# Performance work log

Hardware: AMD Instinct MI355X
Metric: run time of the kernel (lower is better)

The kernel has to match this reference:

```python
import jax, jax.numpy as jnp
import numpy as np

KS = (7, 7)
ST = (3, 3)
PD = (3, 3)
DIM = 512
HID = 1960  # 40 * 49, divisible by kernel_shape


def _patch_flat_idx(out_h, out_w):
    kh, kw = KS; sh, sw = ST; ph, pw = PD
    oh = (out_h + 2 * ph - kh) // sh + 1
    ow = (out_w + 2 * pw - kw) // sw + 1
    Wp = out_w + 2 * pw
    iy = jnp.arange(kh)[:, None, None, None] + (jnp.arange(oh) * sh)[None, None, :, None]
    ix = jnp.arange(kw)[None, :, None, None] + (jnp.arange(ow) * sw)[None, None, None, :]
    # (kh, kw, oh, ow) flat index into padded image
    return (iy * Wp + ix), oh, ow


def fold(patches, out_h, out_w):
    # patches: (B, C*kh*kw, L) -> (B, C, out_h, out_w), overlap-add like F.fold
    kh, kw = KS; ph, pw = PD
    idx, oh, ow = _patch_flat_idx(out_h, out_w)
    B, CK, L = patches.shape
    C = CK // (kh * kw)
    Hp, Wp = out_h + 2 * ph, out_w + 2 * pw
    p = patches.reshape(B, C, kh, kw, oh, ow)
    out = jnp.zeros((B, C, Hp * Wp), patches.dtype)
    out = out.at[:, :, idx.reshape(-1)].add(p.reshape(B, C, -1))
    return out.reshape(B, C, Hp, Wp)[:, :, ph:ph + out_h, pw:pw + out_w]


def unfold(img, out_h, out_w):
    # img: (B, C, H, W) -> (B, C*kh*kw, L), like F.unfold
    kh, kw = KS; ph, pw = PD
    idx, oh, ow = _patch_flat_idx(out_h, out_w)
    B, C = img.shape[:2]
    imgp = jnp.pad(img, ((0, 0), (0, 0), (ph, ph), (pw, pw)))
    flat = imgp.reshape(B, C, -1)
    g = flat[:, :, idx.reshape(-1)].reshape(B, C, kh, kw, oh, ow)
    return g.reshape(B, C * kh * kw, oh * ow)


def setup_inputs() -> dict:
    key = jax.random.key(0)
    k1, k2, k3, k4, k5 = jax.random.split(key, 5)
    x = jax.random.normal(k1, (2, 5760, DIM), dtype=jnp.float32)
    W1 = jax.random.normal(k2, (HID, DIM), dtype=jnp.float32) * 0.02
    b1 = jax.random.normal(k3, (HID,), dtype=jnp.float32) * 0.02
    W2 = jax.random.normal(k4, (DIM, HID), dtype=jnp.float32) * 0.02
    b2 = jax.random.normal(k5, (DIM,), dtype=jnp.float32) * 0.02
    return {"x": x, "W1": W1, "b1": b1, "W2": W2, "b2": b2, "out_h": 60, "out_w": 108}


def reference(x, W1, b1, W2, b2, out_h, out_w):
    kh, kw = KS; sh, sw = ST; ph, pw = PD
    oh = (out_h + 2 * ph - kh) // sh + 1
    ow = (out_w + 2 * pw - kw) // sw + 1
    n_vecs = oh * ow
    h = jnp.einsum('bnd,hd->bnh', x, W1) + b1          # (b, n, HID)
    b_, n, c = h.shape
    p = h.reshape(-1, n_vecs, c).transpose(0, 2, 1)     # (B', c, L)
    folded = fold(p, out_h, out_w)                      # (B', c//49, H, W)
    ones = jnp.ones((p.shape[0], kh * kw, n_vecs), h.dtype)
    norm = fold(ones, out_h, out_w)                     # (B', 1, H, W)
    y = unfold(folded / norm, out_h, out_w)             # (B', c, L)
    y = y.transpose(0, 2, 1).reshape(b_, n, c)
    out = jnp.einsum('bnh,dh->bnd', jax.nn.gelu(y, approximate=False), W2) + b2
    return out
```

## Files before the change

### kernel.cpp

```cpp
#include <hip/hip_runtime.h>
#include <cmath>

#define M_ROWS   11520
#define DIM      512
#define HID      1960
#define HIDP     2048
#define KP2      1984
#define OH       20
#define OW       36
#define LVEC     720
#define NCH      40
#define BPRIME   16
#define HP       66
#define WP       114

typedef unsigned short u16;
typedef __bf16 bf16x8 __attribute__((ext_vector_type(8)));
typedef float  f32x4  __attribute__((ext_vector_type(4)));

__device__ __forceinline__ u16 f2bf(float f) {
    unsigned u = __float_as_uint(f);
    u += 0x7fffu + ((u >> 16) & 1u);
    return (u16)(u >> 16);
}
__device__ __forceinline__ float bf2f(u16 h) {
    return __uint_as_float(((unsigned)h) << 16);
}

__device__ __forceinline__ void gload_lds16(const void* g, void* l) {
    __builtin_amdgcn_global_load_lds(
        (const __attribute__((address_space(1))) void*)g,
        (__attribute__((address_space(3))) void*)l, 16, 0, 0);
}

#define CVT_XB   5760
#define CVT_W1B  1024
#define CVT_W2B  1024
#define CVT_Z    270
__global__ __launch_bounds__(256) void cvt_all(const float* __restrict__ x,
                                               const float* __restrict__ W1,
                                               const float* __restrict__ W2,
                                               u16* __restrict__ xb,
                                               u16* __restrict__ W1b,
                                               u16* __restrict__ W2b,
                                               u16* __restrict__ g2) {
    const int b = blockIdx.x;
    const int tid = threadIdx.x;
    ushort4 o;
    if (b < CVT_XB) {
        int i = (b * 256 + tid) * 4;
        float4 v = *(const float4*)(x + i);
        o.x = f2bf(v.x); o.y = f2bf(v.y); o.z = f2bf(v.z); o.w = f2bf(v.w);
        *(ushort4*)(xb + i) = o;
    } else if (b < CVT_XB + CVT_W1B) {
        int i = ((b - CVT_XB) * 256 + tid) * 4;
        if (i < HID * DIM) {
            float4 v = *(const float4*)(W1 + i);
            o.x = f2bf(v.x); o.y = f2bf(v.y); o.z = f2bf(v.z); o.w = f2bf(v.w);
        } else {
            o.x = o.y = o.z = o.w = 0;
        }
        *(ushort4*)(W1b + i) = o;
    } else if (b < CVT_XB + CVT_W1B + CVT_W2B) {
        int i = ((b - CVT_XB - CVT_W1B) * 256 + tid) * 4;
        int d = i / HIDP, c = i - d * HIDP;
        if (c < HID) {
            float4 v = *(const float4*)(W2 + (size_t)d * HID + c);
            o.x = f2bf(v.x); o.y = f2bf(v.y); o.z = f2bf(v.z); o.w = f2bf(v.w);
        } else {
            o.x = o.y = o.z = o.w = 0;
        }
        *(ushort4*)(W2b + i) = o;
    } else {
        int i = ((b - CVT_XB - CVT_W1B - CVT_W2B) * 256 + tid) * 4;
        int row = i / 24, c = i - row * 24;
        o.x = o.y = o.z = o.w = 0;
        *(ushort4*)(g2 + (size_t)row * HIDP + HID + c) = o;
    }
}

template <int OUT_BF16, int BM, int BN>
__global__ __launch_bounds__(512) void gemm_bt(const u16* __restrict__ A,
                                               const u16* __restrict__ B,
                                               const float* __restrict__ bias,
                                               int biasN, void* __restrict__ Cout,
                                               int N, int K, int ldk) {
    constexpr int WM = BM / 4;
    constexpr int WN = BN / 2;
    constexpr int MU = WM / 16;
    constexpr int NU = WN / 16;
    constexpr int ACH = BM * 8;
    constexpr int BCH = BN * 8;

    __shared__ u16 sA[BM * 64];
    __shared__ u16 sB[BN * 64];

    const int tid  = threadIdx.x;
    const int ntn  = N / BN;
    const int NB   = gridDim.x;
    const int v    = (blockIdx.x & 7) * (NB >> 3) + (blockIdx.x >> 3);
    const int bm   = v / ntn;
    const int bn   = v - bm * ntn;
    const int lane = tid & 63;
    const int wv   = tid >> 6;
    const int wm   = (wv >> 1) * WM;
    const int wn   = (wv & 1) * WN;
    const int r    = lane & 15;
    const int quad = lane >> 4;

    const size_t Arow0 = (size_t)bm * BM * ldk;
    const size_t Brow0 = (size_t)bn * BN * ldk;

    f32x4 acc[MU][NU] = {};

    for (int kt = 0; kt < K; kt += 64) {
        __syncthreads();
#pragma unroll
        for (int i = 0; i < ACH / 512; i++) {
            int e   = i * 512 + tid;
            int row = e >> 3;
            int cp  = e & 7;
            int cg  = cp ^ (row & 7);
            gload_lds16(A + Arow0 + (size_t)row * ldk + kt + cg * 8, (char*)sA + e * 16);
        }
#pragma unroll
        for (int i = 0; i < BCH / 512; i++) {
            int e   = i * 512 + tid;
            int row = e >> 3;
            int cp  = e & 7;
            int cg  = cp ^ (row & 7);
            gload_lds16(B + Brow0 + (size_t)row * ldk + kt + cg * 8, (char*)sB + e * 16);
        }
        __syncthreads();
#pragma unroll
        for (int kk = 0; kk < 2; kk++) {
            bf16x8 af[MU], bg[NU];
#pragma unroll
            for (int t = 0; t < MU; t++) {
                int row = wm + t * 16 + r;
                int c   = (kk * 4 + quad) ^ (row & 7);
                af[t] = *(const bf16x8*)(sA + row * 64 + c * 8);
            }
#pragma unroll
            for (int u = 0; u < NU; u++) {
                int row = wn + u * 16 + r;
                int c   = (kk * 4 + quad) ^ (row & 7);
                bg[u] = *(const bf16x8*)(sB + row * 64 + c * 8);
            }
#pragma unroll
            for (int t = 0; t < MU; t++)
#pragma unroll
                for (int u = 0; u < NU; u++)
                    acc[t][u] = __builtin_amdgcn_mfma_f32_16x16x32_bf16(
                        af[t], bg[u], acc[t][u], 0, 0, 0);
        }
    }

    const int gm0 = bm * BM + wm;
    const int gn0 = bn * BN + wn;
#pragma unroll
    for (int u = 0; u < NU; u++) {
        int gn = gn0 + u * 16 + r;
        float bv = (gn < biasN) ? bias[gn] : 0.0f;
#pragma unroll
        for (int t = 0; t < MU; t++) {
            int gm = gm0 + t * 16 + quad * 4;
#pragma unroll
            for (int q = 0; q < 4; q++) {
                float v2 = acc[t][u][q] + bv;
                if (OUT_BF16)
                    ((u16*)Cout)[(size_t)(gm + q) * N + gn] = f2bf(v2);
                else
                    ((float*)Cout)[(size_t)(gm + q) * N + gn] = v2;
            }
        }
    }
}

__global__ __launch_bounds__(512) void mid_fused(const u16* __restrict__ hg,
                                                 u16* __restrict__ g2) {
    __shared__ u16 sh[12 * 20 * 56];
    __shared__ u16 sG[34 * 58];

    const int b   = blockIdx.x;
    const int bp  = b / (NCH * 4);
    const int rr  = b - bp * (NCH * 4);
    const int ch  = rr >> 2;
    const int s   = (rr >> 1) & 1;
    const int xh  = rr & 1;
    const int o0  = s * 10;
    const int lo  = s * 8;
    const int ox0 = xh * 16;
    const int n0  = bp * LVEC;
    const int c0  = ch * 49;
    const int c0f = c0 & ~7;
    const int koff = c0 & 7;
    const int tid = threadIdx.x;

    {
        const char* hb = (const char*)(hg + (size_t)(n0 + lo * 36 + ox0) * HIDP + c0f);
        for (int t = tid; t < 12 * 20 * 7; t += 512) {
            int r   = (int)(((unsigned)t * 74899u) >> 19);
            int c   = t - r * 7;
            int loy = (int)(((unsigned)r * 3277u) >> 16);
            int oxl = r - 20 * loy;
            gload_lds16(hb + (size_t)(loy * 36 + oxl) * (HIDP * 2) + c * 16,
                        (char*)sh + t * 16);
        }
    }
    __syncthreads();

    const int pxl = tid & 63;
    const int rg  = tid >> 6;
    if (pxl < 58) {
        const int  pxg  = pxl + 54 * xh;
        const bool pxin = (pxg >= 3) && (pxg <= 110);
        const int  kx0  = pxg % 3;
        int  ct[3];
        bool vx[3];
        int  cx = 0;
#pragma unroll
        for (int dx = 0; dx < 3; dx++) {
            int kx = kx0 + 3 * dx, rx = pxg - kx;
            bool ok = pxin && (kx <= 6) && (rx >= 0) && (rx <= 105);
            vx[dx] = ok;
            ct[dx] = ok ? ((rx / 3) - ox0) * 56 + kx : 0;
            cx += ok ? 1 : 0;
        }
        const float fcx = (cx == 3) ? (1.0f / 3.0f) : ((cx == 2) ? 0.5f : 1.0f);

        for (int pr = rg; pr < 34; pr += 8) {
            int py = 3 * o0 + pr;
            float val = 0.0f;
            if (pxin && py >= 3 && py <= 62) {
                int ky0 = py % 3;
                float sum = 0.0f;
                int cy = 0;
#pragma unroll
                for (int dy = 0; dy < 3; dy++) {
                    int ky = ky0 + 3 * dy, ry = py - ky;
                    if (ky <= 6 && ry >= 0 && ry <= 57) {
                        int rt = (ry / 3 - lo) * (20 * 56) + ky * 7 + koff;
                        cy++;
                        float v0 = bf2f(sh[rt + ct[0]]);
                        float v1 = bf2f(sh[rt + ct[1]]);
                        float v2 = bf2f(sh[rt + ct[2]]);
                        sum += vx[0] ? v0 : 0.0f;
                        sum += vx[1] ? v1 : 0.0f;
                        sum += vx[2] ? v2 : 0.0f;
                    }
                }
                float fcy = (cy == 3) ? (1.0f / 3.0f) : ((cy == 2) ? 0.5f : 1.0f);
                float m = sum * fcx * fcy;
                val = 0.5f * m * (1.0f + erff(m * 0.70710678118654752f));
            }
            sG[pr * 58 + pxl] = f2bf(val);
        }
    }
    __syncthreads();

    {
        u16* g2row = g2 + (size_t)(n0 + o0 * 36 + 18 * xh) * HIDP + c0;
        for (int j = tid; j < 10 * 18 * 49; j += 512) {
            int l2 = (int)(((unsigned)j * 42800u) >> 21);
            int k  = j - l2 * 49;
            int oy = (int)(((unsigned)l2 * 57u) >> 10);
            int ox = l2 - 18 * oy;
            int ky = (int)(((unsigned)k * 37u) >> 8);
            int kx = k - 7 * ky;
            g2row[(size_t)(oy * 36 + ox) * HIDP + k] =
                sG[(3 * oy + ky) * 58 + 3 * ox + kx];
        }
    }
}

extern "C" void kernel_launch(void* const* d_in, const int* in_sizes, int n_in,
                              void* d_out, int out_size, void* d_ws, size_t ws_size,
                              hipStream_t stream) {
    (void)in_sizes; (void)n_in; (void)out_size; (void)ws_size;
    const float* x  = (const float*)d_in[0];
    const float* W1 = (const float*)d_in[1];
    const float* b1 = (const float*)d_in[2];
    const float* W2 = (const float*)d_in[3];
    const float* b2 = (const float*)d_in[4];
    float* out = (float*)d_out;

    char* ws = (char*)d_ws;
    u16* xb  = (u16*)(ws);
    u16* W1b = (u16*)(ws + 11796480);
    u16* W2b = (u16*)(ws + 13893632);
    u16* hg  = (u16*)(ws + 15990784);
    u16* g2  = (u16*)(ws + 63176704);

    cvt_all<<<CVT_XB + CVT_W1B + CVT_W2B + CVT_Z, 256, 0, stream>>>(
        x, W1, W2, xb, W1b, W2b, g2);

    gemm_bt<1, 256, 128><<<(M_ROWS / 256) * (HIDP / 128), 512, 0, stream>>>(
        xb, W1b, b1, HID, (void*)hg, HIDP, DIM, DIM);

    mid_fused<<<BPRIME * NCH * 4, 512, 0, stream>>>(hg, g2);

    gemm_bt<0, 128, 64><<<(M_ROWS / 128) * (DIM / 64), 512, 0, stream>>>(
        g2, W2b, b2, DIM, (void*)out, DIM, KP2, HIDP);
}
```

Before: 191.7 us.

## Pipeline GEMM tile loads with a triple-buffered LDS ring and staged bf16 stores

Replaces the single-buffered GEMM with a three-slot LDS ring that issues global-to-LDS loads two tiles ahead and uses explicit vmcnt waits, so loads overlap MFMA work. The first GEMM switches to a BK=32 tile with a different XOR swizzle, and the second keeps BK=64. The bf16 output path now goes through an LDS bounce buffer so each thread writes 16-byte vector stores instead of scattered 2-byte ones. The costs are more LDS per block, hand-counted vmcnt values that assume exactly three loads per thread, and an added occupancy hint in the launch bounds.

```diff
diff --git a/kernel.cpp b/kernel.cpp
--- a/kernel.cpp
+++ b/kernel.cpp
@@ -17,6 +17,7 @@
 typedef unsigned short u16;
 typedef __bf16 bf16x8 __attribute__((ext_vector_type(8)));
 typedef float  f32x4  __attribute__((ext_vector_type(4)));
+typedef unsigned short u16x8 __attribute__((ext_vector_type(8)));
 
 __device__ __forceinline__ u16 f2bf(float f) {
     unsigned u = __float_as_uint(f);
@@ -31,6 +32,12 @@
     __builtin_amdgcn_global_load_lds(
         (const __attribute__((address_space(1))) void*)g,
         (__attribute__((address_space(3))) void*)l, 16, 0, 0);
+}
+
+__device__ __forceinline__ void wg_barrier() {
+    asm volatile("" ::: "memory");
+    __builtin_amdgcn_s_barrier();
+    asm volatile("" ::: "memory");
 }
 
 #define CVT_XB   5760
@@ -79,21 +86,25 @@
     }
 }
 
-template <int OUT_BF16, int BM, int BN>
-__global__ __launch_bounds__(512) void gemm_bt(const u16* __restrict__ A,
-                                               const u16* __restrict__ B,
-                                               const float* __restrict__ bias,
-                                               int biasN, void* __restrict__ Cout,
-                                               int N, int K, int ldk) {
-    constexpr int WM = BM / 4;
-    constexpr int WN = BN / 2;
-    constexpr int MU = WM / 16;
-    constexpr int NU = WN / 16;
-    constexpr int ACH = BM * 8;
-    constexpr int BCH = BN * 8;
-
-    __shared__ u16 sA[BM * 64];
-    __shared__ u16 sB[BN * 64];
+template <int OUT_BF16, int BM, int BN, int BK>
+__global__ __launch_bounds__(512, 4) void gemm_ring(const u16* __restrict__ A,
+                                                    const u16* __restrict__ B,
+                                                    const float* __restrict__ bias,
+                                                    int biasN, void* __restrict__ Cout,
+                                                    int N, int K, int ldk) {
+    constexpr int WM  = BM / 4;
+    constexpr int WN  = BN / 2;
+    constexpr int MU  = WM / 16;
+    constexpr int NU  = WN / 16;
+    constexpr int KB  = BK / 32;
+    constexpr int CPR = BK / 8;
+    constexpr int CA  = BM * CPR;
+    constexpr int CB  = BN * CPR;
+    constexpr int TILEU = (BM + BN) * BK;
+    static_assert(CA % 512 == 0 && CB % 512 == 0, "chunk split");
+    static_assert(CA / 512 + CB / 512 == 3, "need 3 loads/thread for vmcnt(6/3/0)");
+
+    __shared__ u16 smem[3 * TILEU];
 
     const int tid  = threadIdx.x;
     const int ntn  = N / BN;
@@ -110,68 +121,114 @@
 
     const size_t Arow0 = (size_t)bm * BM * ldk;
     const size_t Brow0 = (size_t)bn * BN * ldk;
+    const int NT = K / BK;
+
+    auto issue = [&](int t) {
+        const size_t kt = (size_t)t * BK;
+        u16* sa = smem + (t % 3) * TILEU;
+        u16* sb = sa + BM * BK;
+#pragma unroll
+        for (int i = 0; i < CA / 512; i++) {
+            int e   = i * 512 + tid;
+            int row = e / CPR;
+            int cp  = e % CPR;
+            int key = (BK == 64) ? (row & 7) : ((row >> 1) & 3);
+            gload_lds16(A + Arow0 + (size_t)row * ldk + kt + (size_t)((cp ^ key) * 8),
+                        (char*)sa + e * 16);
+        }
+#pragma unroll
+        for (int i = 0; i < CB / 512; i++) {
+            int e   = i * 512 + tid;
+            int row = e / CPR;
+            int cp  = e % CPR;
+            int key = (BK == 64) ? (row & 7) : ((row >> 1) & 3);
+            gload_lds16(B + Brow0 + (size_t)row * ldk + kt + (size_t)((cp ^ key) * 8),
+                        (char*)sb + e * 16);
+        }
+    };
+
+    issue(0);
+    issue(1);
 
     f32x4 acc[MU][NU] = {};
 
-    for (int kt = 0; kt < K; kt += 64) {
-        __syncthreads();
-#pragma unroll
-        for (int i = 0; i < ACH / 512; i++) {
-            int e   = i * 512 + tid;
-            int row = e >> 3;
-            int cp  = e & 7;
-            int cg  = cp ^ (row & 7);
-            gload_lds16(A + Arow0 + (size_t)row * ldk + kt + cg * 8, (char*)sA + e * 16);
-        }
-#pragma unroll
-        for (int i = 0; i < BCH / 512; i++) {
-            int e   = i * 512 + tid;
-            int row = e >> 3;
-            int cp  = e & 7;
-            int cg  = cp ^ (row & 7);
-            gload_lds16(B + Brow0 + (size_t)row * ldk + kt + cg * 8, (char*)sB + e * 16);
-        }
-        __syncthreads();
-#pragma unroll
-        for (int kk = 0; kk < 2; kk++) {
+    for (int t = 0; t < NT; ++t) {
+        if (t + 2 < NT) issue(t + 2);
+        if (t + 2 < NT)      asm volatile("s_waitcnt vmcnt(6)" ::: "memory");
+        else if (t + 1 < NT) asm volatile("s_waitcnt vmcnt(3)" ::: "memory");
+        else                 asm volatile("s_waitcnt vmcnt(0)" ::: "memory");
+        wg_barrier();
+
+        const u16* sa = smem + (t % 3) * TILEU;
+        const u16* sb = sa + BM * BK;
+#pragma unroll
+        for (int kk = 0; kk < KB; kk++) {
             bf16x8 af[MU], bg[NU];
 #pragma unroll
-            for (int t = 0; t < MU; t++) {
-                int row = wm + t * 16 + r;
-                int c   = (kk * 4 + quad) ^ (row & 7);
-                af[t] = *(const bf16x8*)(sA + row * 64 + c * 8);
+            for (int m = 0; m < MU; m++) {
+                int row = wm + m * 16 + r;
+                int key = (BK == 64) ? (row & 7) : ((row >> 1) & 3);
+                int c   = (kk * 4 + quad) ^ key;
+                af[m] = *(const bf16x8*)(sa + row * BK + c * 8);
             }
 #pragma unroll
             for (int u = 0; u < NU; u++) {
                 int row = wn + u * 16 + r;
-                int c   = (kk * 4 + quad) ^ (row & 7);
-                bg[u] = *(const bf16x8*)(sB + row * 64 + c * 8);
-            }
-#pragma unroll
-            for (int t = 0; t < MU; t++)
+                int key = (BK == 64) ? (row & 7) : ((row >> 1) & 3);
+                int c   = (kk * 4 + quad) ^ key;
+                bg[u] = *(const bf16x8*)(sb + row * BK + c * 8);
+            }
+#pragma unroll
+            for (int m = 0; m < MU; m++)
 #pragma unroll
                 for (int u = 0; u < NU; u++)
-                    acc[t][u] = __builtin_amdgcn_mfma_f32_16x16x32_bf16(
-                        af[t], bg[u], acc[t][u], 0, 0, 0);
-        }
-    }
-
-    const int gm0 = bm * BM + wm;
-    const int gn0 = bn * BN + wn;
-#pragma unroll
-    for (int u = 0; u < NU; u++) {
-        int gn = gn0 + u * 16 + r;
-        float bv = (gn < biasN) ? bias[gn] : 0.0f;
-#pragma unroll
-        for (int t = 0; t < MU; t++) {
-            int gm = gm0 + t * 16 + quad * 4;
-#pragma unroll
-            for (int q = 0; q < 4; q++) {
-                float v2 = acc[t][u][q] + bv;
-                if (OUT_BF16)
-                    ((u16*)Cout)[(size_t)(gm + q) * N + gn] = f2bf(v2);
-                else
-                    ((float*)Cout)[(size_t)(gm + q) * N + gn] = v2;
+                    acc[m][u] = __builtin_amdgcn_mfma_f32_16x16x32_bf16(
+                        af[m], bg[u], acc[m][u], 0, 0, 0);
+        }
+        wg_barrier();
+    }
+
+    if constexpr (OUT_BF16) {
+        constexpr int LDC = BN + 8;
+        static_assert(BM * LDC <= 3 * TILEU, "bounce fits in ring LDS");
+        static_assert(BM == 256 && BN == 128, "store split assumes 256x128");
+        u16* sC = smem;
+#pragma unroll
+        for (int u = 0; u < NU; u++) {
+            int gnl = wn + u * 16 + r;
+            int gng = bn * BN + gnl;
+            float bv = (gng < biasN) ? bias[gng] : 0.0f;
+#pragma unroll
+            for (int m = 0; m < MU; m++) {
+                int gml = wm + m * 16 + quad * 4;
+#pragma unroll
+                for (int q = 0; q < 4; q++)
+                    sC[(gml + q) * LDC + gnl] = f2bf(acc[m][u][q] + bv);
+            }
+        }
+        wg_barrier();
+        const int row  = tid >> 1;
+        const int half = tid & 1;
+        const size_t gb = (size_t)(bm * BM + row) * N + bn * BN + half * 64;
+        const u16* src = sC + row * LDC + half * 64;
+#pragma unroll
+        for (int j = 0; j < 8; j++) {
+            u16x8 w = *(const u16x8*)(src + j * 8);
+            *(u16x8*)((u16*)Cout + gb + j * 8) = w;
+        }
+    } else {
+        const int gm0 = bm * BM + wm;
+        const int gn0 = bn * BN + wn;
+#pragma unroll
+        for (int u = 0; u < NU; u++) {
+            int gn = gn0 + u * 16 + r;
+            float bv = (gn < biasN) ? bias[gn] : 0.0f;
+#pragma unroll
+            for (int m = 0; m < MU; m++) {
+                int gm = gm0 + m * 16 + quad * 4;
+#pragma unroll
+                for (int q = 0; q < 4; q++)
+                    ((float*)Cout)[(size_t)(gm + q) * N + gn] = acc[m][u][q] + bv;
             }
         }
     }
@@ -295,11 +352,11 @@
     cvt_all<<<CVT_XB + CVT_W1B + CVT_W2B + CVT_Z, 256, 0, stream>>>(
         x, W1, W2, xb, W1b, W2b, g2);
 
-    gemm_bt<1, 256, 128><<<(M_ROWS / 256) * (HIDP / 128), 512, 0, stream>>>(
+    gemm_ring<1, 256, 128, 32><<<(M_ROWS / 256) * (HIDP / 128), 512, 0, stream>>>(
         xb, W1b, b1, HID, (void*)hg, HIDP, DIM, DIM);
 
     mid_fused<<<BPRIME * NCH * 4, 512, 0, stream>>>(hg, g2);
 
-    gemm_bt<0, 128, 64><<<(M_ROWS / 128) * (DIM / 64), 512, 0, stream>>>(
+    gemm_ring<0, 128, 64, 64><<<(M_ROWS / 128) * (DIM / 64), 512, 0, stream>>>(
         g2, W2b, b2, DIM, (void*)out, DIM, KP2, HIDP);
 }
```

Result: slower. 204.3 us (+6.5%).
